# Kernel optimization log

Measured on AMD Instinct MI355X. Metric: run time of the kernel, lower is better.

The kernel has to match this reference:

```python
import jax, jax.numpy as jnp
import numpy as np

D_MODEL = 1024
N_HEADS = 16
D_KEY = 64
ALIBI_SLOPE = 8.0
B, S = 2, 2048


def setup_inputs() -> dict:
    key = jax.random.key(0)
    ks = jax.random.split(key, 10)
    sd = D_MODEL ** -0.5
    states = jax.random.normal(ks[0], (B, S, D_MODEL), dtype=jnp.float32)
    bias_mask = jax.random.normal(ks[1], (B, S, S), dtype=jnp.float32)
    # non-trainable ALiBi-style per-head scale
    head_scale = jnp.exp2(-((jnp.arange(N_HEADS, dtype=jnp.float32) + 1.0) * ALIBI_SLOPE / N_HEADS))
    # parameters (torch Linear: y = x @ W.T + b)
    Wa = jax.random.normal(ks[2], (N_HEADS, D_MODEL), dtype=jnp.float32) * sd  # a_proj, no bias
    Wv = jax.random.normal(ks[3], (D_MODEL, D_MODEL), dtype=jnp.float32) * sd
    bv = jnp.zeros((D_MODEL,), dtype=jnp.float32)
    Wg = jax.random.normal(ks[4], (N_HEADS, D_MODEL), dtype=jnp.float32) * sd
    bg = jnp.zeros((N_HEADS,), dtype=jnp.float32)
    Wo = jax.random.normal(ks[5], (D_MODEL, D_MODEL), dtype=jnp.float32) * sd
    bo = jnp.zeros((D_MODEL,), dtype=jnp.float32)
    return {"states": states, "bias_mask": bias_mask, "head_scale": head_scale,
            "Wa": Wa, "Wv": Wv, "bv": bv, "Wg": Wg, "bg": bg, "Wo": Wo, "bo": bo}


def reference(states, bias_mask, head_scale, Wa, Wv, bv, Wg, bg, Wo, bo):
    # bias: [B,1,Q,K] * [1,H,1,1] -> [B,H,Q,K]
    bias = bias_mask[:, None, :, :] * head_scale[None, :, None, None]
    # values: [B,K,H,dk]
    v = (jnp.einsum('bkm,dm->bkd', states, Wv) + bv).reshape(states.shape[0], states.shape[1], N_HEADS, D_KEY)
    # key-only scores: [B,S,H] -> [B,H,1,K], plus bias -> [B,H,Q,K]
    a = jnp.einsum('bkm,hm->bhk', states, Wa)[:, :, None, :] + bias
    a = jax.nn.softmax(a, axis=-1)
    o = jnp.einsum('bhqk,bkhd->bqhd', a, v)
    g = jnp.einsum('bqm,hm->bqh', states, Wg) + bg
    o = o * jax.nn.sigmoid(g)[..., None]
    o = o.reshape(o.shape[0], o.shape[1], D_MODEL)
    return jnp.einsum('bqm,dm->bqd', o, Wo) + bo
```

## Files before the change

### kernel.cpp

```cpp
#include <hip/hip_runtime.h>


#define LOG2E 1.44269504088896f

using f16   = _Float16;
using f16x4 = __attribute__((ext_vector_type(4))) _Float16;
using f16x8 = __attribute__((ext_vector_type(8))) _Float16;
using f32x4 = __attribute__((ext_vector_type(4))) float;

#define GLDS16(g, l) __builtin_amdgcn_global_load_lds((const __attribute__((address_space(1))) void*)(g), (__attribute__((address_space(3))) void*)(l), 16, 0, 0)

__global__ __launch_bounds__(256) void k_prep(
    const float* __restrict__ states, const float* __restrict__ mask,
    const float* __restrict__ Wa, const float* __restrict__ Wv,
    const float* __restrict__ Wg, const float* __restrict__ Wo,
    f16* __restrict__ st16, f16* __restrict__ Wv16, f16* __restrict__ Wo16,
    f16* __restrict__ Wag16)
{
  const int bid = blockIdx.x;
  const int t   = threadIdx.x;
  if (bid < 1024) {
    const int row = bid * 4 + (t >> 6);
    const int lane = t & 63;
    const float* sp = states + (size_t)row * 1024 + lane * 16;
    float4 v0 = ((const float4*)sp)[0];
    float4 v1 = ((const float4*)sp)[1];
    float4 v2 = ((const float4*)sp)[2];
    float4 v3 = ((const float4*)sp)[3];
    f16x8 h0, h1;
    h0[0]=(f16)v0.x; h0[1]=(f16)v0.y; h0[2]=(f16)v0.z; h0[3]=(f16)v0.w;
    h0[4]=(f16)v1.x; h0[5]=(f16)v1.y; h0[6]=(f16)v1.z; h0[7]=(f16)v1.w;
    h1[0]=(f16)v2.x; h1[1]=(f16)v2.y; h1[2]=(f16)v2.z; h1[3]=(f16)v2.w;
    h1[4]=(f16)v3.x; h1[5]=(f16)v3.y; h1[6]=(f16)v3.z; h1[7]=(f16)v3.w;
    f16* dp = st16 + (size_t)row * 1024 + lane * 16;
    *(f16x8*)dp = h0; *(f16x8*)(dp + 8) = h1;
  } else {
    const int cb = bid - 1024;
    {
      int idx = cb * 2048 + t * 8;
      const float* src; f16* dst;
      if (idx < 1048576)      { src = Wv + idx;             dst = Wv16 + idx; }
      else if (idx < 2097152) { src = Wo + (idx - 1048576); dst = Wo16 + (idx - 1048576); }
      else { int j = idx - 2097152;
             src = (j < 16384) ? (Wa + j) : (Wg + (j - 16384));
             dst = Wag16 + j; }
      float4 v0 = ((const float4*)src)[0];
      float4 v1 = ((const float4*)src)[1];
      f16x8 h;
      h[0]=(f16)v0.x; h[1]=(f16)v0.y; h[2]=(f16)v0.z; h[3]=(f16)v0.w;
      h[4]=(f16)v1.x; h[5]=(f16)v1.y; h[6]=(f16)v1.z; h[7]=(f16)v1.w;
      *(f16x8*)dst = h;
    }
    if (cb < 512) {
      const float4* mp = (const float4*)(mask + (size_t)cb * 16384);
      float sx = 0.f, sy = 0.f, sz = 0.f, sw = 0.f;
      #pragma unroll
      for (int i = 0; i < 16; ++i) {
        float4 v = mp[t + i * 256];
        sx += v.x; sy += v.y; sz += v.z; sw += v.w;
      }
      asm volatile("" :: "v"(sx), "v"(sy), "v"(sz), "v"(sw));
    }
  }
}

__global__ __launch_bounds__(256) void k_vg(
    const f16* __restrict__ A, const f16* __restrict__ Bw,
    const float* __restrict__ bv, f16* __restrict__ vt,
    const f16* __restrict__ Bag, const float* __restrict__ bg,
    f16* __restrict__ s16, float* __restrict__ gsig, float* __restrict__ partialS)
{
  __shared__ f16 As[2 * 4096], Bs[2 * 2048];
  const int t = threadIdx.x, wid = t >> 6, lane = t & 63;
  const int lane15 = lane & 15, lg = lane >> 4;
  const int sswz = ((t & 3) ^ ((t >> 3) & 3)) * 8;

  if (blockIdx.x < 32) {
    const int bi = blockIdx.x;
    const int r0 = bi * 128;
    const int b  = bi >> 4;
    const int wm = wid >> 1, wn = wid & 1;
    f32x4 acc[4] = {};
    const f16* ga0 = A  + (size_t)(r0 + (t >> 2)) * 1024      + sswz;
    const f16* ga1 = A  + (size_t)(r0 + 64 + (t >> 2)) * 1024 + sswz;
    const f16* gb0 = Bag + (size_t)(t >> 2) * 1024            + sswz;
    int ra[4], rb;
    #pragma unroll
    for (int m = 0; m < 4; ++m) { int r_ = wm*64 + m*16 + lane15; ra[m] = r_*32 + ((lg ^ ((r_>>1)&3)) * 8); }
    { int r_ = wn*16 + lane15; rb = r_*32 + ((lg ^ ((r_>>1)&3)) * 8); }

    #define STAGE_SG(kt, bb) do { const int k0_ = (kt) * 32; \
        GLDS16(ga0 + k0_, As + (bb)*4096 + wid*512); \
        GLDS16(ga1 + k0_, As + (bb)*4096 + 2048 + wid*512); \
        if (wid < 2) GLDS16(gb0 + k0_, Bs + (bb)*1024 + wid*512); } while(0)
    STAGE_SG(0, 0);
    for (int kt = 0; kt < 32; ++kt) {
      const int cur = kt & 1;
      if (kt < 31) {
        STAGE_SG(kt + 1, cur ^ 1);
        if (wid < 2) asm volatile("s_waitcnt vmcnt(3)" ::: "memory");
        else         asm volatile("s_waitcnt vmcnt(2)" ::: "memory");
      } else {
        asm volatile("s_waitcnt vmcnt(0)" ::: "memory");
      }
      __builtin_amdgcn_s_barrier();
      f16x8 a[4], bf;
      #pragma unroll
      for (int m = 0; m < 4; ++m) a[m] = *(const f16x8*)(As + cur*4096 + ra[m]);
      bf = *(const f16x8*)(Bs + cur*1024 + rb);
      #pragma unroll
      for (int m = 0; m < 4; ++m)
        acc[m] = __builtin_amdgcn_mfma_f32_16x16x32_f16(a[m], bf, acc[m], 0, 0, 0);
      asm volatile("s_waitcnt lgkmcnt(0)" ::: "memory");
      __builtin_amdgcn_s_barrier();
    }
    #undef STAGE_SG
    const int c = wn * 16 + lane15;
    if (wn == 0) {
      float mx = -1e30f;
      #pragma unroll
      for (int m = 0; m < 4; ++m) {
        const int q0 = (r0 & 2047) + wm * 64 + m * 16 + lg * 4;
        f16x4 hv;
        #pragma unroll
        for (int r = 0; r < 4; ++r) { mx = fmaxf(mx, acc[m][r]); hv[r] = (f16)acc[m][r]; }
        *(f16x4*)(s16 + (size_t)(b * 16 + c) * 2048 + q0) = hv;
      }
      mx = fmaxf(mx, __shfl_xor(mx, 16, 64));
      mx = fmaxf(mx, __shfl_xor(mx, 32, 64));
      if (lg == 0) partialS[(bi * 2 + wm) * 16 + c] = mx;
    } else {
      const float bgv = bg[c - 16];
      #pragma unroll
      for (int m = 0; m < 4; ++m) {
        const int q0 = (r0 & 2047) + wm * 64 + m * 16 + lg * 4;
        #pragma unroll
        for (int r = 0; r < 4; ++r) {
          const float g = acc[m][r] + bgv;
          gsig[(size_t)(b * 2048 + q0 + r) * 16 + (c - 16)] = 1.f / (1.f + __expf(-g));
        }
      }
    }
    return;
  }

  const int p = blockIdx.x - 32;
  const int l = (p & 7) * 64 + (p >> 3);
  const int r0 = (l >> 4) * 128, n0 = (l & 15) * 64;
  const int wr = wid >> 1, wc = wid & 1;
  f32x4 acc[4][2] = {};
  const f16* ga0 = A  + (size_t)(r0 + (t >> 2)) * 1024       + sswz;
  const f16* ga1 = A  + (size_t)(r0 + 64 + (t >> 2)) * 1024  + sswz;
  const f16* gb0 = Bw + (size_t)(n0 + (t >> 2)) * 1024       + sswz;
  int ra[4], rb[2];
  #pragma unroll
  for (int m = 0; m < 4; ++m) { int r_ = wr*64 + m*16 + lane15; ra[m] = r_*32 + ((lg ^ ((r_>>1)&3)) * 8); }
  #pragma unroll
  for (int n = 0; n < 2; ++n) { int r_ = wc*32 + n*16 + lane15; rb[n] = r_*32 + ((lg ^ ((r_>>1)&3)) * 8); }

  #define STAGE_G(kt, bb) do { const int k0_ = (kt) * 32; \
      GLDS16(ga0 + k0_, As + (bb)*4096 + wid*512); \
      GLDS16(ga1 + k0_, As + (bb)*4096 + 2048 + wid*512); \
      GLDS16(gb0 + k0_, Bs + (bb)*2048 + wid*512); } while(0)
  STAGE_G(0, 0);
  for (int kt = 0; kt < 32; ++kt) {
    const int cur = kt & 1;
    if (kt < 31) {
      STAGE_G(kt + 1, cur ^ 1);
      asm volatile("s_waitcnt vmcnt(3)" ::: "memory");
    } else {
      asm volatile("s_waitcnt vmcnt(0)" ::: "memory");
    }
    __builtin_amdgcn_s_barrier();
    f16x8 a[4], bf[2];
    #pragma unroll
    for (int m = 0; m < 4; ++m) a[m] = *(const f16x8*)(As + cur*4096 + ra[m]);
    #pragma unroll
    for (int n = 0; n < 2; ++n) bf[n] = *(const f16x8*)(Bs + cur*2048 + rb[n]);
    #pragma unroll
    for (int m = 0; m < 4; ++m)
      #pragma unroll
      for (int n = 0; n < 2; ++n)
        acc[m][n] = __builtin_amdgcn_mfma_f32_16x16x32_f16(a[m], bf[n], acc[m][n], 0, 0, 0);
    asm volatile("s_waitcnt lgkmcnt(0)" ::: "memory");
    __builtin_amdgcn_s_barrier();
  }
  #undef STAGE_G
  const int b_ = r0 >> 11;
  #pragma unroll
  for (int n = 0; n < 2; ++n) {
    const int gn = n0 + wc * 32 + n * 16 + lane15;
    const float bvv = bv[gn];
    #pragma unroll
    for (int m = 0; m < 4; ++m) {
      const int kb = (r0 & 2047) + wr * 64 + m * 16 + lg * 4;
      f16x4 hv;
      #pragma unroll
      for (int r = 0; r < 4; ++r) hv[r] = (f16)(acc[m][n][r] + bvv);
      *(f16x4*)(vt + (size_t)(b_ * 1024 + gn) * 2048 + kb) = hv;
    }
  }
}

__global__ __launch_bounds__(256, 4) void k_attn(
    const float* __restrict__ mask, const f16* __restrict__ s16,
    const float* __restrict__ gsig, const float* __restrict__ hs,
    const float* __restrict__ partialS, const f16* __restrict__ vt,
    f16* __restrict__ og)
{
  __shared__ __align__(16) f16 mks[2 * 4096];
  __shared__ __align__(16) f16 vs[2 * 4096];

  const int p = blockIdx.x;
  const int l = (p & 7) * 128 + (p >> 3);
  const int b = l >> 9, rr = l & 511;
  const int qt = rr >> 4, h = rr & 15;

  const int t = threadIdx.x, wid = t >> 6, lane = t & 63;
  const int lane15 = lane & 15, lg = lane >> 4;

  const int l31 = lane & 31;
  float mxs = partialS[b * 512 + (l31 >> 1) * 32 + (l31 & 1) * 16 + h];
  #pragma unroll
  for (int off = 16; off; off >>= 1) mxs = fmaxf(mxs, __shfl_xor(mxs, off, 64));
  const float hsv = hs[h];
  const float L   = mxs + hsv * 8.0f;
  const float c2  = hsv * LOG2E;
  const float nLc = -L * LOG2E;

  const f16* vtb = vt + (size_t)(b * 1024 + h * 64) * 2048;
  const int q16 = wid * 16 + lane15;

  const int mrow = t >> 2;
  const float* msrc = mask + (size_t)b * 4194304 + (size_t)(qt * 64 + mrow) * 2048 + (t & 3) * 16;
  const f16* sptr = s16 + (size_t)(b * 16 + h) * 2048 + lg * 8;

  const int mw0 = mrow * 64 + ((((t & 3) * 2    ) ^ (mrow & 7)) * 8);
  const int mw1 = mrow * 64 + ((((t & 3) * 2 + 1) ^ (mrow & 7)) * 8);
  const int mr0 = q16 * 64 + (((    lg) ^ (q16 & 7)) * 8);
  const int mr1 = q16 * 64 + (((4 + lg) ^ (q16 & 7)) * 8);

  const int vswz = ((t & 7) ^ ((t >> 3) & 7)) * 8;
  const f16* vsrc0 = vtb + (size_t)(     (t >> 3)) * 2048 + vswz;
  const f16* vsrc1 = vtb + (size_t)(32 + (t >> 3)) * 2048 + vswz;
  int voff[2][4];
  #pragma unroll
  for (int kk = 0; kk < 2; ++kk)
    #pragma unroll
    for (int n = 0; n < 4; ++n)
      voff[kk][n] = (n * 16 + lane15) * 64 + (((kk * 4 + lg) ^ (lane15 & 7)) * 8);

  f32x4 acc[4] = {};
  float den = 0.f;
  f32x4 mg0, mg1, mg2, mg3;

  #define MLOAD(KV) do { \
    mg0 = *(const f32x4*)(msrc + (KV));      mg1 = *(const f32x4*)(msrc + (KV) + 4); \
    mg2 = *(const f32x4*)(msrc + (KV) + 8);  mg3 = *(const f32x4*)(msrc + (KV) + 12); } while (0)

  #define MWRITE(BB) do { \
    f16x8 h0_, h1_; \
    h0_[0]=(f16)mg0[0]; h0_[1]=(f16)mg0[1]; h0_[2]=(f16)mg0[2]; h0_[3]=(f16)mg0[3]; \
    h0_[4]=(f16)mg1[0]; h0_[5]=(f16)mg1[1]; h0_[6]=(f16)mg1[2]; h0_[7]=(f16)mg1[3]; \
    h1_[0]=(f16)mg2[0]; h1_[1]=(f16)mg2[1]; h1_[2]=(f16)mg2[2]; h1_[3]=(f16)mg2[3]; \
    h1_[4]=(f16)mg3[0]; h1_[5]=(f16)mg3[1]; h1_[6]=(f16)mg3[2]; h1_[7]=(f16)mg3[3]; \
    *(f16x8*)(mks + (BB)*4096 + mw0) = h0_; \
    *(f16x8*)(mks + (BB)*4096 + mw1) = h1_; } while (0)

  #define STAGE_V(KV, BB) do { \
    GLDS16(vsrc0 + (KV), vs + (BB)*4096 +        wid*512); \
    GLDS16(vsrc1 + (KV), vs + (BB)*4096 + 2048 + wid*512); } while (0)

  #define KKBODY(KK, SH, CUR) do { \
    f16x8 mh = *(const f16x8*)(mks + (CUR)*4096 + ((KK) ? mr1 : mr0)); \
    f16x8 vf0 = *(const f16x8*)(vs + (CUR)*4096 + voff[KK][0]); \
    f16x8 vf1 = *(const f16x8*)(vs + (CUR)*4096 + voff[KK][1]); \
    f16x8 vf2 = *(const f16x8*)(vs + (CUR)*4096 + voff[KK][2]); \
    f16x8 vf3 = *(const f16x8*)(vs + (CUR)*4096 + voff[KK][3]); \
    f16x8 af; float dl_ = 0.f; \
    _Pragma("unroll") \
    for (int j_ = 0; j_ < 8; ++j_) { \
      float sxj = fmaf((float)SH[j_], LOG2E, nLc); \
      float w_ = __builtin_amdgcn_exp2f(fmaf(c2, (float)mh[j_], sxj)); \
      dl_ += w_; af[j_] = (f16)w_; \
    } \
    den += dl_; \
    acc[0] = __builtin_amdgcn_mfma_f32_16x16x32_f16(af, vf0, acc[0], 0, 0, 0); \
    acc[1] = __builtin_amdgcn_mfma_f32_16x16x32_f16(af, vf1, acc[1], 0, 0, 0); \
    acc[2] = __builtin_amdgcn_mfma_f32_16x16x32_f16(af, vf2, acc[2], 0, 0, 0); \
    acc[3] = __builtin_amdgcn_mfma_f32_16x16x32_f16(af, vf3, acc[3], 0, 0, 0); } while (0)

  MLOAD(0);
  STAGE_V(0, 0);
  asm volatile("s_waitcnt vmcnt(2)" ::: "memory");
  MWRITE(0);
  asm volatile("s_waitcnt lgkmcnt(0)" ::: "memory");

  #pragma unroll 1
  for (int kt = 0; kt < 32; ++kt) {
    const int kv = kt * 64;
    const int cur = kt & 1;
    f16x8 s0r = *(const f16x8*)(sptr + kv);
    f16x8 s1r = *(const f16x8*)(sptr + kv + 32);
    if (kt < 31) {
      MLOAD(kv + 64);
      STAGE_V(kv + 64, cur ^ 1);
      asm volatile("s_waitcnt vmcnt(8)" ::: "memory");
    } else {
      asm volatile("s_waitcnt vmcnt(2)" ::: "memory");
    }
    __builtin_amdgcn_s_barrier();
    __builtin_amdgcn_s_setprio(1);
    KKBODY(0, s0r, cur);
    KKBODY(1, s1r, cur);
    __builtin_amdgcn_s_setprio(0);
    if (kt < 31) {
      asm volatile("s_waitcnt vmcnt(2)" ::: "memory");
      MWRITE(cur ^ 1);
    }
    asm volatile("s_waitcnt lgkmcnt(0)" ::: "memory");
    __builtin_amdgcn_s_barrier();
  }
  #undef KKBODY
  #undef STAGE_V
  #undef MWRITE
  #undef MLOAD

  den += __shfl_xor(den, 16, 64);
  den += __shfl_xor(den, 32, 64);

  #pragma unroll
  for (int r = 0; r < 4; ++r) {
    const int ql = lg * 4 + r;
    const int q = qt * 64 + wid * 16 + ql;
    const float dq = __shfl(den, ql, 64);
    const float sc = gsig[(size_t)(b * 2048 + q) * 16 + h] / dq;
    #pragma unroll
    for (int n = 0; n < 4; ++n)
      og[(size_t)(b * 2048 + q) * 1024 + h * 64 + n * 16 + lane15] = (f16)(acc[n][r] * sc);
  }
}

__global__ __launch_bounds__(256) void k_gemm_out(
    const f16* __restrict__ A, const f16* __restrict__ Bw,
    const float* __restrict__ bo, float* __restrict__ out)
{
  __shared__ f16 As[2 * 4096], Bs[2 * 2048];
  const int p = blockIdx.x;
  const int l = (p & 7) * 64 + (p >> 3);
  const int r0 = (l >> 4) * 128, n0 = (l & 15) * 64;
  const int t = threadIdx.x, wid = t >> 6, lane = t & 63;
  const int lane15 = lane & 15, lg = lane >> 4;
  const int wr = wid >> 1, wc = wid & 1;
  f32x4 acc[4][2] = {};
  const int sswz = ((t & 3) ^ ((t >> 3) & 3)) * 8;
  const f16* ga0 = A  + (size_t)(r0 + (t >> 2)) * 1024       + sswz;
  const f16* ga1 = A  + (size_t)(r0 + 64 + (t >> 2)) * 1024  + sswz;
  const f16* gb0 = Bw + (size_t)(n0 + (t >> 2)) * 1024       + sswz;
  int ra[4], rb[2];
  #pragma unroll
  for (int m = 0; m < 4; ++m) { int r_ = wr*64 + m*16 + lane15; ra[m] = r_*32 + ((lg ^ ((r_>>1)&3)) * 8); }
  #pragma unroll
  for (int n = 0; n < 2; ++n) { int r_ = wc*32 + n*16 + lane15; rb[n] = r_*32 + ((lg ^ ((r_>>1)&3)) * 8); }

  #define STAGE_G(kt, bb) do { const int k0_ = (kt) * 32; \
      GLDS16(ga0 + k0_, As + (bb)*4096 + wid*512); \
      GLDS16(ga1 + k0_, As + (bb)*4096 + 2048 + wid*512); \
      GLDS16(gb0 + k0_, Bs + (bb)*2048 + wid*512); } while(0)
  STAGE_G(0, 0);
  for (int kt = 0; kt < 32; ++kt) {
    const int cur = kt & 1;
    if (kt < 31) {
      STAGE_G(kt + 1, cur ^ 1);
      asm volatile("s_waitcnt vmcnt(3)" ::: "memory");
    } else {
      asm volatile("s_waitcnt vmcnt(0)" ::: "memory");
    }
    __builtin_amdgcn_s_barrier();
    f16x8 a[4], bf[2];
    #pragma unroll
    for (int m = 0; m < 4; ++m) a[m] = *(const f16x8*)(As + cur*4096 + ra[m]);
    #pragma unroll
    for (int n = 0; n < 2; ++n) bf[n] = *(const f16x8*)(Bs + cur*2048 + rb[n]);
    #pragma unroll
    for (int m = 0; m < 4; ++m)
      #pragma unroll
      for (int n = 0; n < 2; ++n)
        acc[m][n] = __builtin_amdgcn_mfma_f32_16x16x32_f16(a[m], bf[n], acc[m][n], 0, 0, 0);
    asm volatile("s_waitcnt lgkmcnt(0)" ::: "memory");
    __builtin_amdgcn_s_barrier();
  }
  #undef STAGE_G
  #pragma unroll
  for (int n = 0; n < 2; ++n) {
    const int gn = n0 + wc * 32 + n * 16 + lane15;
    const float bov = bo[gn];
    #pragma unroll
    for (int m = 0; m < 4; ++m) {
      const int rbase = r0 + wr * 64 + m * 16 + lg * 4;
      #pragma unroll
      for (int r = 0; r < 4; ++r)
        out[(size_t)(rbase + r) * 1024 + gn] = acc[m][n][r] + bov;
    }
  }
}

extern "C" void kernel_launch(void* const* d_in, const int* in_sizes, int n_in,
                              void* d_out, int out_size, void* d_ws, size_t ws_size,
                              hipStream_t stream)
{
  const float* states = (const float*)d_in[0];
  const float* mask   = (const float*)d_in[1];
  const float* hs     = (const float*)d_in[2];
  const float* Wa     = (const float*)d_in[3];
  const float* Wv     = (const float*)d_in[4];
  const float* bv     = (const float*)d_in[5];
  const float* Wg     = (const float*)d_in[6];
  const float* bg     = (const float*)d_in[7];
  const float* Wo     = (const float*)d_in[8];
  const float* bo     = (const float*)d_in[9];
  float* out = (float*)d_out;

  char* ws = (char*)d_ws;
  f16*   st16     = (f16*)(ws);
  f16*   og       = (f16*)(ws);
  f16*   Wv16     = (f16*)(ws + 8388608);
  f16*   Wo16     = (f16*)(ws + 10485760);
  f16*   Wag16    = (f16*)(ws + 12582912);
  float* gsig     = (float*)(ws + 12648448);
  f16*   s16      = (f16*)(ws + 12910592);
  float* partialS = (float*)(ws + 13043712);
  f16*   vt       = (f16*)(ws + 13107200);

  k_prep<<<2064, 256, 0, stream>>>(states, mask, Wa, Wv, Wg, Wo,
                                   st16, Wv16, Wo16, Wag16);
  k_vg<<<544, 256, 0, stream>>>(st16, Wv16, bv, vt, Wag16, bg, s16, gsig, partialS);
  k_attn<<<1024, 256, 0, stream>>>(mask, s16, gsig, hs, partialS, vt, og);
  k_gemm_out<<<512, 256, 0, stream>>>(og, Wo16, bo, out);
}
```

Before: 118.1 us.

## Stage fp32 mask via direct global-to-LDS loads and read V straight into registers

The attention kernel now copies the fp32 bias mask straight into a swizzled LDS buffer with global_load_lds. This replaces the old path that loaded it into registers, converted it to fp16 and wrote it to LDS. V tiles are no longer staged through LDS; each lane loads its MFMA operands directly from global memory, one tile ahead. The mask cache-warming reads move from the prep kernel into extra blocks of the V/gate GEMM kernel so they overlap with that work. In exchange, LDS traffic per tile is larger because the mask stays fp32, and the V loads from global memory are uncoalesced per-lane reads.

```diff
diff --git a/kernel.cpp b/kernel.cpp
--- a/kernel.cpp
+++ b/kernel.cpp
@@ -11,7 +11,7 @@
 #define GLDS16(g, l) __builtin_amdgcn_global_load_lds((const __attribute__((address_space(1))) void*)(g), (__attribute__((address_space(3))) void*)(l), 16, 0, 0)
 
 __global__ __launch_bounds__(256) void k_prep(
-    const float* __restrict__ states, const float* __restrict__ mask,
+    const float* __restrict__ states,
     const float* __restrict__ Wa, const float* __restrict__ Wv,
     const float* __restrict__ Wg, const float* __restrict__ Wo,
     f16* __restrict__ st16, f16* __restrict__ Wv16, f16* __restrict__ Wo16,
@@ -36,31 +36,19 @@
     *(f16x8*)dp = h0; *(f16x8*)(dp + 8) = h1;
   } else {
     const int cb = bid - 1024;
-    {
-      int idx = cb * 2048 + t * 8;
-      const float* src; f16* dst;
-      if (idx < 1048576)      { src = Wv + idx;             dst = Wv16 + idx; }
-      else if (idx < 2097152) { src = Wo + (idx - 1048576); dst = Wo16 + (idx - 1048576); }
-      else { int j = idx - 2097152;
-             src = (j < 16384) ? (Wa + j) : (Wg + (j - 16384));
-             dst = Wag16 + j; }
-      float4 v0 = ((const float4*)src)[0];
-      float4 v1 = ((const float4*)src)[1];
-      f16x8 h;
-      h[0]=(f16)v0.x; h[1]=(f16)v0.y; h[2]=(f16)v0.z; h[3]=(f16)v0.w;
-      h[4]=(f16)v1.x; h[5]=(f16)v1.y; h[6]=(f16)v1.z; h[7]=(f16)v1.w;
-      *(f16x8*)dst = h;
-    }
-    if (cb < 512) {
-      const float4* mp = (const float4*)(mask + (size_t)cb * 16384);
-      float sx = 0.f, sy = 0.f, sz = 0.f, sw = 0.f;
-      #pragma unroll
-      for (int i = 0; i < 16; ++i) {
-        float4 v = mp[t + i * 256];
-        sx += v.x; sy += v.y; sz += v.z; sw += v.w;
-      }
-      asm volatile("" :: "v"(sx), "v"(sy), "v"(sz), "v"(sw));
-    }
+    int idx = cb * 2048 + t * 8;
+    const float* src; f16* dst;
+    if (idx < 1048576)      { src = Wv + idx;             dst = Wv16 + idx; }
+    else if (idx < 2097152) { src = Wo + (idx - 1048576); dst = Wo16 + (idx - 1048576); }
+    else { int j = idx - 2097152;
+           src = (j < 16384) ? (Wa + j) : (Wg + (j - 16384));
+           dst = Wag16 + j; }
+    float4 v0 = ((const float4*)src)[0];
+    float4 v1 = ((const float4*)src)[1];
+    f16x8 h;
+    h[0]=(f16)v0.x; h[1]=(f16)v0.y; h[2]=(f16)v0.z; h[3]=(f16)v0.w;
+    h[4]=(f16)v1.x; h[5]=(f16)v1.y; h[6]=(f16)v1.z; h[7]=(f16)v1.w;
+    *(f16x8*)dst = h;
   }
 }
 
@@ -68,8 +56,23 @@
     const f16* __restrict__ A, const f16* __restrict__ Bw,
     const float* __restrict__ bv, f16* __restrict__ vt,
     const f16* __restrict__ Bag, const float* __restrict__ bg,
-    f16* __restrict__ s16, float* __restrict__ gsig, float* __restrict__ partialS)
+    f16* __restrict__ s16, float* __restrict__ gsig, float* __restrict__ partialS,
+    const float* __restrict__ mask)
 {
+  if (blockIdx.x >= 544) {
+    const int cb = blockIdx.x - 544;
+    const int t = threadIdx.x;
+    const float4* mp = (const float4*)(mask + (size_t)cb * 16384);
+    float sx = 0.f, sy = 0.f, sz = 0.f, sw = 0.f;
+    #pragma unroll
+    for (int i = 0; i < 16; ++i) {
+      float4 v = mp[t + i * 256];
+      sx += v.x; sy += v.y; sz += v.z; sw += v.w;
+    }
+    asm volatile("" :: "v"(sx), "v"(sy), "v"(sz), "v"(sw));
+    return;
+  }
+
   __shared__ f16 As[2 * 4096], Bs[2 * 2048];
   const int t = threadIdx.x, wid = t >> 6, lane = t & 63;
   const int lane15 = lane & 15, lg = lane >> 4;
@@ -208,8 +211,7 @@
     const float* __restrict__ partialS, const f16* __restrict__ vt,
     f16* __restrict__ og)
 {
-  __shared__ __align__(16) f16 mks[2 * 4096];
-  __shared__ __align__(16) f16 vs[2 * 4096];
+  __shared__ __align__(16) float mk[2 * 4096];
 
   const int p = blockIdx.x;
   const int l = (p & 7) * 128 + (p >> 3);
@@ -228,73 +230,70 @@
   const float c2  = hsv * LOG2E;
   const float nLc = -L * LOG2E;
 
-  const f16* vtb = vt + (size_t)(b * 1024 + h * 64) * 2048;
   const int q16 = wid * 16 + lane15;
-
-  const int mrow = t >> 2;
-  const float* msrc = mask + (size_t)b * 4194304 + (size_t)(qt * 64 + mrow) * 2048 + (t & 3) * 16;
+  const float* mbase = mask + (size_t)b * 4194304 + (size_t)(qt * 64) * 2048;
+
+  const int mswz = ((t & 15) ^ ((t >> 4) & 7)) * 4;
+  const float* msrc0 = mbase + (size_t)(     (t >> 4)) * 2048 + mswz;
+  const float* msrc1 = mbase + (size_t)(16 + (t >> 4)) * 2048 + mswz;
+  const float* msrc2 = mbase + (size_t)(32 + (t >> 4)) * 2048 + mswz;
+  const float* msrc3 = mbase + (size_t)(48 + (t >> 4)) * 2048 + mswz;
+
+  int moff[2][2];
+  #pragma unroll
+  for (int kk = 0; kk < 2; ++kk) {
+    const int sl = kk * 8 + lg * 2;
+    moff[kk][0] = q16 * 64 + ((sl    ) ^ (q16 & 7)) * 4;
+    moff[kk][1] = q16 * 64 + ((sl + 1) ^ (q16 & 7)) * 4;
+  }
+
   const f16* sptr = s16 + (size_t)(b * 16 + h) * 2048 + lg * 8;
 
-  const int mw0 = mrow * 64 + ((((t & 3) * 2    ) ^ (mrow & 7)) * 8);
-  const int mw1 = mrow * 64 + ((((t & 3) * 2 + 1) ^ (mrow & 7)) * 8);
-  const int mr0 = q16 * 64 + (((    lg) ^ (q16 & 7)) * 8);
-  const int mr1 = q16 * 64 + (((4 + lg) ^ (q16 & 7)) * 8);
-
-  const int vswz = ((t & 7) ^ ((t >> 3) & 7)) * 8;
-  const f16* vsrc0 = vtb + (size_t)(     (t >> 3)) * 2048 + vswz;
-  const f16* vsrc1 = vtb + (size_t)(32 + (t >> 3)) * 2048 + vswz;
-  int voff[2][4];
-  #pragma unroll
-  for (int kk = 0; kk < 2; ++kk)
-    #pragma unroll
-    for (int n = 0; n < 4; ++n)
-      voff[kk][n] = (n * 16 + lane15) * 64 + (((kk * 4 + lg) ^ (lane15 & 7)) * 8);
+  const f16* vpb = vt + (size_t)(b * 1024 + h * 64 + lane15) * 2048 + lg * 8;
+  const f16* vp0 = vpb;
+  const f16* vp1 = vpb + 16 * 2048;
+  const f16* vp2 = vpb + 32 * 2048;
+  const f16* vp3 = vpb + 48 * 2048;
 
   f32x4 acc[4] = {};
   float den = 0.f;
-  f32x4 mg0, mg1, mg2, mg3;
-
-  #define MLOAD(KV) do { \
-    mg0 = *(const f32x4*)(msrc + (KV));      mg1 = *(const f32x4*)(msrc + (KV) + 4); \
-    mg2 = *(const f32x4*)(msrc + (KV) + 8);  mg3 = *(const f32x4*)(msrc + (KV) + 12); } while (0)
-
-  #define MWRITE(BB) do { \
-    f16x8 h0_, h1_; \
-    h0_[0]=(f16)mg0[0]; h0_[1]=(f16)mg0[1]; h0_[2]=(f16)mg0[2]; h0_[3]=(f16)mg0[3]; \
-    h0_[4]=(f16)mg1[0]; h0_[5]=(f16)mg1[1]; h0_[6]=(f16)mg1[2]; h0_[7]=(f16)mg1[3]; \
-    h1_[0]=(f16)mg2[0]; h1_[1]=(f16)mg2[1]; h1_[2]=(f16)mg2[2]; h1_[3]=(f16)mg2[3]; \
-    h1_[4]=(f16)mg3[0]; h1_[5]=(f16)mg3[1]; h1_[6]=(f16)mg3[2]; h1_[7]=(f16)mg3[3]; \
-    *(f16x8*)(mks + (BB)*4096 + mw0) = h0_; \
-    *(f16x8*)(mks + (BB)*4096 + mw1) = h1_; } while (0)
-
-  #define STAGE_V(KV, BB) do { \
-    GLDS16(vsrc0 + (KV), vs + (BB)*4096 +        wid*512); \
-    GLDS16(vsrc1 + (KV), vs + (BB)*4096 + 2048 + wid*512); } while (0)
-
-  #define KKBODY(KK, SH, CUR) do { \
-    f16x8 mh = *(const f16x8*)(mks + (CUR)*4096 + ((KK) ? mr1 : mr0)); \
-    f16x8 vf0 = *(const f16x8*)(vs + (CUR)*4096 + voff[KK][0]); \
-    f16x8 vf1 = *(const f16x8*)(vs + (CUR)*4096 + voff[KK][1]); \
-    f16x8 vf2 = *(const f16x8*)(vs + (CUR)*4096 + voff[KK][2]); \
-    f16x8 vf3 = *(const f16x8*)(vs + (CUR)*4096 + voff[KK][3]); \
-    f16x8 af; float dl_ = 0.f; \
-    _Pragma("unroll") \
-    for (int j_ = 0; j_ < 8; ++j_) { \
-      float sxj = fmaf((float)SH[j_], LOG2E, nLc); \
-      float w_ = __builtin_amdgcn_exp2f(fmaf(c2, (float)mh[j_], sxj)); \
-      dl_ += w_; af[j_] = (f16)w_; \
-    } \
+  f16x8 v00, v01, v10, v11, v20, v21, v30, v31;
+
+  #define MSTAGE(KV, BB) do { \
+    GLDS16(msrc0 + (KV), mk + (BB)*4096 +        wid*256); \
+    GLDS16(msrc1 + (KV), mk + (BB)*4096 + 1024 + wid*256); \
+    GLDS16(msrc2 + (KV), mk + (BB)*4096 + 2048 + wid*256); \
+    GLDS16(msrc3 + (KV), mk + (BB)*4096 + 3072 + wid*256); } while (0)
+
+  #define VLOAD(KV) do { \
+    v00 = *(const f16x8*)(vp0 + (KV)); v01 = *(const f16x8*)(vp0 + (KV) + 32); \
+    v10 = *(const f16x8*)(vp1 + (KV)); v11 = *(const f16x8*)(vp1 + (KV) + 32); \
+    v20 = *(const f16x8*)(vp2 + (KV)); v21 = *(const f16x8*)(vp2 + (KV) + 32); \
+    v30 = *(const f16x8*)(vp3 + (KV)); v31 = *(const f16x8*)(vp3 + (KV) + 32); } while (0)
+
+  #define KKBODY(KK, SH, MKC, VF0, VF1, VF2, VF3) do { \
+    f32x4 ma = *(const f32x4*)((MKC) + moff[KK][0]); \
+    f32x4 mb = *(const f32x4*)((MKC) + moff[KK][1]); \
+    f16x8 af; float dl_; \
+    float w0 = __builtin_amdgcn_exp2f(fmaf(c2, ma[0], fmaf((float)SH[0], LOG2E, nLc))); \
+    float w1 = __builtin_amdgcn_exp2f(fmaf(c2, ma[1], fmaf((float)SH[1], LOG2E, nLc))); \
+    float w2 = __builtin_amdgcn_exp2f(fmaf(c2, ma[2], fmaf((float)SH[2], LOG2E, nLc))); \
+    float w3 = __builtin_amdgcn_exp2f(fmaf(c2, ma[3], fmaf((float)SH[3], LOG2E, nLc))); \
+    float w4 = __builtin_amdgcn_exp2f(fmaf(c2, mb[0], fmaf((float)SH[4], LOG2E, nLc))); \
+    float w5 = __builtin_amdgcn_exp2f(fmaf(c2, mb[1], fmaf((float)SH[5], LOG2E, nLc))); \
+    float w6 = __builtin_amdgcn_exp2f(fmaf(c2, mb[2], fmaf((float)SH[6], LOG2E, nLc))); \
+    float w7 = __builtin_amdgcn_exp2f(fmaf(c2, mb[3], fmaf((float)SH[7], LOG2E, nLc))); \
+    af[0]=(f16)w0; af[1]=(f16)w1; af[2]=(f16)w2; af[3]=(f16)w3; \
+    af[4]=(f16)w4; af[5]=(f16)w5; af[6]=(f16)w6; af[7]=(f16)w7; \
+    dl_ = ((w0 + w1) + (w2 + w3)) + ((w4 + w5) + (w6 + w7)); \
     den += dl_; \
-    acc[0] = __builtin_amdgcn_mfma_f32_16x16x32_f16(af, vf0, acc[0], 0, 0, 0); \
-    acc[1] = __builtin_amdgcn_mfma_f32_16x16x32_f16(af, vf1, acc[1], 0, 0, 0); \
-    acc[2] = __builtin_amdgcn_mfma_f32_16x16x32_f16(af, vf2, acc[2], 0, 0, 0); \
-    acc[3] = __builtin_amdgcn_mfma_f32_16x16x32_f16(af, vf3, acc[3], 0, 0, 0); } while (0)
-
-  MLOAD(0);
-  STAGE_V(0, 0);
-  asm volatile("s_waitcnt vmcnt(2)" ::: "memory");
-  MWRITE(0);
-  asm volatile("s_waitcnt lgkmcnt(0)" ::: "memory");
+    acc[0] = __builtin_amdgcn_mfma_f32_16x16x32_f16(af, VF0, acc[0], 0, 0, 0); \
+    acc[1] = __builtin_amdgcn_mfma_f32_16x16x32_f16(af, VF1, acc[1], 0, 0, 0); \
+    acc[2] = __builtin_amdgcn_mfma_f32_16x16x32_f16(af, VF2, acc[2], 0, 0, 0); \
+    acc[3] = __builtin_amdgcn_mfma_f32_16x16x32_f16(af, VF3, acc[3], 0, 0, 0); } while (0)
+
+  MSTAGE(0, 0);
+  VLOAD(0);
 
   #pragma unroll 1
   for (int kt = 0; kt < 32; ++kt) {
@@ -303,28 +302,24 @@
     f16x8 s0r = *(const f16x8*)(sptr + kv);
     f16x8 s1r = *(const f16x8*)(sptr + kv + 32);
     if (kt < 31) {
-      MLOAD(kv + 64);
-      STAGE_V(kv + 64, cur ^ 1);
-      asm volatile("s_waitcnt vmcnt(8)" ::: "memory");
+      MSTAGE(kv + 64, cur ^ 1);
+      asm volatile("s_waitcnt vmcnt(4)" ::: "memory");
     } else {
-      asm volatile("s_waitcnt vmcnt(2)" ::: "memory");
+      asm volatile("s_waitcnt vmcnt(0)" ::: "memory");
     }
     __builtin_amdgcn_s_barrier();
     __builtin_amdgcn_s_setprio(1);
-    KKBODY(0, s0r, cur);
-    KKBODY(1, s1r, cur);
+    const float* mkc = mk + cur * 4096;
+    KKBODY(0, s0r, mkc, v00, v10, v20, v30);
+    KKBODY(1, s1r, mkc, v01, v11, v21, v31);
     __builtin_amdgcn_s_setprio(0);
-    if (kt < 31) {
-      asm volatile("s_waitcnt vmcnt(2)" ::: "memory");
-      MWRITE(cur ^ 1);
-    }
+    if (kt < 31) VLOAD(kv + 64);
     asm volatile("s_waitcnt lgkmcnt(0)" ::: "memory");
     __builtin_amdgcn_s_barrier();
   }
   #undef KKBODY
-  #undef STAGE_V
-  #undef MWRITE
-  #undef MLOAD
+  #undef VLOAD
+  #undef MSTAGE
 
   den += __shfl_xor(den, 16, 64);
   den += __shfl_xor(den, 32, 64);
@@ -432,9 +427,9 @@
   float* partialS = (float*)(ws + 13043712);
   f16*   vt       = (f16*)(ws + 13107200);
 
-  k_prep<<<2064, 256, 0, stream>>>(states, mask, Wa, Wv, Wg, Wo,
+  k_prep<<<2064, 256, 0, stream>>>(states, Wa, Wv, Wg, Wo,
                                    st16, Wv16, Wo16, Wag16);
-  k_vg<<<544, 256, 0, stream>>>(st16, Wv16, bv, vt, Wag16, bg, s16, gsig, partialS);
+  k_vg<<<1056, 256, 0, stream>>>(st16, Wv16, bv, vt, Wag16, bg, s16, gsig, partialS, mask);
   k_attn<<<1024, 256, 0, stream>>>(mask, s16, gsig, hs, partialS, vt, og);
   k_gemm_out<<<512, 256, 0, stream>>>(og, Wo16, bo, out);
 }
```

After: 198.7 us. +68.2%, slower.
